# Performance work log

Hardware: AMD Instinct MI355X
Metric: run time of the kernel (lower is better)

The kernel has to match this reference:

```python
import jax, jax.numpy as jnp
import numpy as np

B, Dx, Dz, Dy, H = 4096, 512, 512, 256, 2048
T0, T1 = 0.0, 1.0
N_STEPS = 64


def setup_inputs() -> dict:
    key = jax.random.key(0)
    ks = jax.random.split(key, 9)
    X = jax.random.normal(ks[0], (B, Dx), jnp.float32)
    # P sampled Uniform(0.01, 0.1) as in the torch module
    P = jax.random.uniform(ks[1], (Dz, Dx), jnp.float32, 0.01, 0.1)
    # A scaled so spectral radius ~1 -> exp(A*T) stays bounded over the integration
    A = jax.random.normal(ks[2], (Dz, Dz), jnp.float32) * (Dz ** -0.5)
    W1 = jax.random.normal(ks[3], (H, Dz), jnp.float32) * (Dz ** -0.5)
    b1 = jax.random.normal(ks[4], (H,), jnp.float32) * 0.01
    W2 = jax.random.normal(ks[5], (H, H), jnp.float32) * (H ** -0.5)
    b2 = jax.random.normal(ks[6], (H,), jnp.float32) * 0.01
    W3 = jax.random.normal(ks[7], (Dy, H), jnp.float32) * (H ** -0.5)
    b3 = jax.random.normal(ks[8], (Dy,), jnp.float32) * 0.01
    return dict(X=X, P=P, A=A, W1=W1, b1=b1, W2=W2, b2=b2, W3=W3, b3=b3,
                n_steps=N_STEPS)


def reference(X, P, A, W1, b1, W2, b2, W3, b3, n_steps):
    # Z0 = einsum('ji,bi->bj', P, X)  -> projection into latent ODE state
    z0 = X @ P.T  # [B, Dz]
    dt = jnp.float32((T1 - T0) / n_steps)

    def f(z):  # dz/dt = A z, batched: einsum('ji,bi->bj', A, z)
        return z @ A.T

    def rk4_step(z, _):
        k1 = f(z)
        k2 = f(z + 0.5 * dt * k1)
        k3 = f(z + 0.5 * dt * k2)
        k4 = f(z + dt * k3)
        return z + (dt / 6.0) * (k1 + 2.0 * k2 + 2.0 * k3 + k4), None

    zT, _ = jax.lax.scan(rk4_step, z0, None, length=n_steps)  # [B, Dz]

    # QnnMatrixODE MLP head (n_layers=3): Lin+ReLU, Lin+ReLU, Lin
    h = jax.nn.relu(zT @ W1.T + b1)
    h = jax.nn.relu(h @ W2.T + b2)
    y = h @ W3.T + b3  # [B, Dy]
    return y
```

## Files before the change

### kernel.cpp

```cpp
#include <hip/hip_runtime.h>

#define BDIM 4096
#define DX 512
#define DZ 512
#define DY 256
#define HD 2048
#define LDT 72

typedef __attribute__((ext_vector_type(8))) short bf16x8;
typedef __attribute__((ext_vector_type(4))) float f32x4;

__device__ inline unsigned short f2bf(float f) {
    unsigned u = __float_as_uint(f);
    unsigned r = 0x7FFFu + ((u >> 16) & 1u);
    return (unsigned short)((u + r) >> 16);
}
__device__ inline float bf2f(unsigned short h) {
    return __uint_as_float(((unsigned)h) << 16);
}

#define GLDS16(g, l)                                                            \
    __builtin_amdgcn_global_load_lds((const __attribute__((address_space(1))) void*)(g), \
                                     (__attribute__((address_space(3))) void*)(l), 16, 0, 0)

struct CvtJobs {
    const float* src[5];
    unsigned short* hi[5];
    unsigned short* lo[5];
    int n4[5];
};
__global__ __launch_bounds__(256) void cvt_multi_k(CvtJobs J) {
    const int j = blockIdx.y;
    const int i4 = blockIdx.x * 256 + threadIdx.x;
    if (i4 >= J.n4[j]) return;
    float4 v = ((const float4*)J.src[j])[i4];
    ushort4 h;
    h.x = f2bf(v.x); h.y = f2bf(v.y); h.z = f2bf(v.z); h.w = f2bf(v.w);
    ((ushort4*)J.hi[j])[i4] = h;
    if (J.lo[j]) {
        ushort4 l;
        l.x = f2bf(v.x - bf2f(h.x));
        l.y = f2bf(v.y - bf2f(h.y));
        l.z = f2bf(v.z - bf2f(h.z));
        l.w = f2bf(v.w - bf2f(h.w));
        ((ushort4*)J.lo[j])[i4] = l;
    }
}

__global__ __launch_bounds__(256) void split_t_k(const float* __restrict__ A0,
                                                 unsigned short* __restrict__ H0,
                                                 unsigned short* __restrict__ L0,
                                                 const float* __restrict__ A1,
                                                 unsigned short* __restrict__ H1,
                                                 unsigned short* __restrict__ L1, int D) {
    const float* A = blockIdx.z ? A1 : A0;
    unsigned short* HT = blockIdx.z ? H1 : H0;
    unsigned short* LT = blockIdx.z ? L1 : L0;
    __shared__ float t[32][33];
    const int bx = blockIdx.x * 32, by = blockIdx.y * 32;
    const int x = threadIdx.x, y = threadIdx.y;
#pragma unroll
    for (int dy = 0; dy < 32; dy += 8)
        t[y + dy][x] = A[(size_t)(by + y + dy) * D + bx + x];
    __syncthreads();
#pragma unroll
    for (int dy = 0; dy < 32; dy += 8) {
        float v = t[x][y + dy];
        unsigned short h = f2bf(v);
        size_t o = (size_t)(bx + y + dy) * D + by + x;
        HT[o] = h;
        LT[o] = f2bf(v - bf2f(h));
    }
}

__global__ __launch_bounds__(256) void e0_k(const float* __restrict__ A,
                                            const float* __restrict__ A2,
                                            const float* __restrict__ A3,
                                            float* __restrict__ B0,
                                            float* __restrict__ B1,
                                            float* __restrict__ B2,
                                            unsigned short* __restrict__ B3h,
                                            unsigned short* __restrict__ B3l) {
    const int i4 = blockIdx.x * 256 + threadIdx.x;
    const int base = i4 * 4;
    const int row = base >> 9, col = base & 511;
    const int d = row - col;
    float4 a = ((const float4*)A)[i4];
    float4 a2 = ((const float4*)A2)[i4];
    float4 a3 = ((const float4*)A3)[i4];
    float av[4] = {a.x, a.y, a.z, a.w};
    float a2v[4] = {a2.x, a2.y, a2.z, a2.w};
    float a3v[4] = {a3.x, a3.y, a3.z, a3.w};
    float b0[4], b1[4], b2[4];
    ushort4 h3, l3;
    unsigned short* h3p = &h3.x;
    unsigned short* l3p = &l3.x;
#pragma unroll
    for (int j = 0; j < 4; ++j) {
        const float di = (j == d) ? 1.0f : 0.0f;
        b0[j] = di + av[j] + 0.5f * a2v[j] + 1.6666667e-1f * a3v[j];
        b1[j] = 4.1666668e-2f * di + 8.3333333e-3f * av[j] +
                1.3888889e-3f * a2v[j] + 1.9841270e-4f * a3v[j];
        b2[j] = 2.4801587e-5f * di + 2.7557319e-6f * av[j] +
                2.7557319e-7f * a2v[j] + 2.5052108e-8f * a3v[j];
        float b3 = 2.0876757e-9f * di + 1.6059044e-10f * av[j] +
                   1.1470746e-11f * a2v[j] + 7.6471637e-13f * a3v[j];
        unsigned short hh = f2bf(b3);
        h3p[j] = hh;
        l3p[j] = f2bf(b3 - bf2f(hh));
    }
    ((float4*)B0)[i4] = make_float4(b0[0], b0[1], b0[2], b0[3]);
    ((float4*)B1)[i4] = make_float4(b1[0], b1[1], b1[2], b1[3]);
    ((float4*)B2)[i4] = make_float4(b2[0], b2[1], b2[2], b2[3]);
    ((ushort4*)B3h)[i4] = h3;
    ((ushort4*)B3l)[i4] = l3;
}

struct G64In { const unsigned short *Ahi, *Alo, *Bhi, *Blo; const float* Dadd; };
struct G64Out { float* Cf32; unsigned short *Chi, *Clo, *CThi, *CTlo; };

__device__ __forceinline__ void g64_core(int bx, int by, int M, int N, int K,
                                         G64In in, G64Out o,
                                         unsigned short* Ash, unsigned short* Asl,
                                         unsigned short* Bsh, unsigned short* Bsl) {
    const int tid = threadIdx.x;
    const int lane = tid & 63;
    const int wave = tid >> 6;
    const int wr = wave >> 1, wc = wave & 1;
    const int row0 = by * 64, col0 = bx * 64;
    const int sr = tid >> 2;
    const int sk = (tid & 3) * 16;

    const int niter = K >> 6;
    bf16x8 pa0, pa1, pl0, pl1, pb0, pb1, pq0, pq1;
    {
        const unsigned short* ar = in.Ahi + (size_t)(row0 + sr) * K + sk;
        const unsigned short* al = in.Alo + (size_t)(row0 + sr) * K + sk;
        const unsigned short* br = in.Bhi + (size_t)(col0 + sr) * K + sk;
        const unsigned short* bl = in.Blo + (size_t)(col0 + sr) * K + sk;
        pa0 = *(const bf16x8*)ar; pa1 = *(const bf16x8*)(ar + 8);
        pl0 = *(const bf16x8*)al; pl1 = *(const bf16x8*)(al + 8);
        pb0 = *(const bf16x8*)br; pb1 = *(const bf16x8*)(br + 8);
        pq0 = *(const bf16x8*)bl; pq1 = *(const bf16x8*)(bl + 8);
    }

    f32x4 acc[4] = {};
    const int mb = wr * 32 + (lane & 15);
    const int nb = wc * 32 + (lane & 15);

    for (int it = 0; it < niter; ++it) {
        __syncthreads();
        *(bf16x8*)&Ash[sr * LDT + sk] = pa0; *(bf16x8*)&Ash[sr * LDT + sk + 8] = pa1;
        *(bf16x8*)&Asl[sr * LDT + sk] = pl0; *(bf16x8*)&Asl[sr * LDT + sk + 8] = pl1;
        *(bf16x8*)&Bsh[sr * LDT + sk] = pb0; *(bf16x8*)&Bsh[sr * LDT + sk + 8] = pb1;
        *(bf16x8*)&Bsl[sr * LDT + sk] = pq0; *(bf16x8*)&Bsl[sr * LDT + sk + 8] = pq1;
        __syncthreads();

        {
            const int kn = (it + 1 < niter) ? ((it + 1) << 6) : 0;
            const unsigned short* ar = in.Ahi + (size_t)(row0 + sr) * K + kn + sk;
            const unsigned short* al = in.Alo + (size_t)(row0 + sr) * K + kn + sk;
            const unsigned short* br = in.Bhi + (size_t)(col0 + sr) * K + kn + sk;
            const unsigned short* bl = in.Blo + (size_t)(col0 + sr) * K + kn + sk;
            pa0 = *(const bf16x8*)ar; pa1 = *(const bf16x8*)(ar + 8);
            pl0 = *(const bf16x8*)al; pl1 = *(const bf16x8*)(al + 8);
            pb0 = *(const bf16x8*)br; pb1 = *(const bf16x8*)(br + 8);
            pq0 = *(const bf16x8*)bl; pq1 = *(const bf16x8*)(bl + 8);
        }

#pragma unroll
        for (int kh = 0; kh < 2; ++kh) {
            const int kk = kh * 32 + (lane >> 4) * 8;
            bf16x8 ah[2], alx[2], bh[2], blx[2];
#pragma unroll
            for (int t = 0; t < 2; ++t) {
                ah[t]  = *(const bf16x8*)&Ash[(mb + t * 16) * LDT + kk];
                alx[t] = *(const bf16x8*)&Asl[(mb + t * 16) * LDT + kk];
                bh[t]  = *(const bf16x8*)&Bsh[(nb + t * 16) * LDT + kk];
                blx[t] = *(const bf16x8*)&Bsl[(nb + t * 16) * LDT + kk];
            }
#pragma unroll
            for (int mt = 0; mt < 2; ++mt)
#pragma unroll
                for (int nt = 0; nt < 2; ++nt) {
                    acc[mt * 2 + nt] = __builtin_amdgcn_mfma_f32_16x16x32_bf16(
                        ah[mt], bh[nt], acc[mt * 2 + nt], 0, 0, 0);
                    acc[mt * 2 + nt] = __builtin_amdgcn_mfma_f32_16x16x32_bf16(
                        ah[mt], blx[nt], acc[mt * 2 + nt], 0, 0, 0);
                    acc[mt * 2 + nt] = __builtin_amdgcn_mfma_f32_16x16x32_bf16(
                        alx[mt], bh[nt], acc[mt * 2 + nt], 0, 0, 0);
                }
        }
    }

#pragma unroll
    for (int mt = 0; mt < 2; ++mt) {
        const int grow = row0 + wr * 32 + mt * 16 + (lane >> 4) * 4;
#pragma unroll
        for (int nt = 0; nt < 2; ++nt) {
            const int gcol = col0 + wc * 32 + nt * 16 + (lane & 15);
            f32x4 a = acc[mt * 2 + nt];
            if (in.Dadd) {
#pragma unroll
                for (int i = 0; i < 4; ++i)
                    a[i] += in.Dadd[(size_t)(grow + i) * N + gcol];
            }
            unsigned short h4[4], l4[4];
#pragma unroll
            for (int i = 0; i < 4; ++i) {
                h4[i] = f2bf(a[i]);
                l4[i] = f2bf(a[i] - bf2f(h4[i]));
            }
            if (o.Cf32) {
#pragma unroll
                for (int i = 0; i < 4; ++i) o.Cf32[(size_t)(grow + i) * N + gcol] = a[i];
            }
            if (o.Chi) {
#pragma unroll
                for (int i = 0; i < 4; ++i) o.Chi[(size_t)(grow + i) * N + gcol] = h4[i];
            }
            if (o.Clo) {
#pragma unroll
                for (int i = 0; i < 4; ++i) o.Clo[(size_t)(grow + i) * N + gcol] = l4[i];
            }
            if (o.CThi) {
                ushort4 u = {h4[0], h4[1], h4[2], h4[3]};
                *(ushort4*)&o.CThi[(size_t)gcol * M + grow] = u;
            }
            if (o.CTlo) {
                ushort4 u = {l4[0], l4[1], l4[2], l4[3]};
                *(ushort4*)&o.CTlo[(size_t)gcol * M + grow] = u;
            }
        }
    }
}

__global__ __launch_bounds__(256) void g64_one(G64In in, G64Out o, int M, int N, int K) {
    __shared__ __align__(16) unsigned short Ash[64 * LDT], Asl[64 * LDT];
    __shared__ __align__(16) unsigned short Bsh[64 * LDT], Bsl[64 * LDT];
    g64_core(blockIdx.x, blockIdx.y, M, N, K, in, o, Ash, Asl, Bsh, Bsl);
}

__global__ __launch_bounds__(256) void g64_dual(G64In i0, G64Out o0, G64In i1, G64Out o1,
                                                int M, int N, int K) {
    __shared__ __align__(16) unsigned short Ash[64 * LDT], Asl[64 * LDT];
    __shared__ __align__(16) unsigned short Bsh[64 * LDT], Bsl[64 * LDT];
    g64_core(blockIdx.x, blockIdx.y, M, N, K, blockIdx.z ? i1 : i0, blockIdx.z ? o1 : o0,
             Ash, Asl, Bsh, Bsl);
}

template <int RELU, int BIAS, int OUT_BF16>
__global__ __launch_bounds__(256) void gemm_bf16_v2(int M, int N, int K,
                                                    const unsigned short* __restrict__ A,
                                                    const unsigned short* __restrict__ B,
                                                    void* __restrict__ C,
                                                    const float* __restrict__ bias) {
    __shared__ unsigned short As[64 * 32];
    __shared__ unsigned short Bs[128 * 32];

    const int tid = threadIdx.x;
    const int lane = tid & 63;
    const int wave = tid >> 6;
    const int wr = wave >> 1, wc = wave & 1;
    const int row0 = blockIdx.y * 64;
    const int col0 = blockIdx.x * 128;

    const int srow = lane >> 2;
    const int schunk = (lane & 3) * 8;

    f32x4 acc[2][4] = {};

    for (int k0 = 0; k0 < K; k0 += 32) {
        GLDS16(A + (size_t)(row0 + wave * 16 + srow) * K + k0 + schunk, &As[(wave * 16) * 32]);
        GLDS16(B + (size_t)(col0 + wave * 32 + srow) * K + k0 + schunk, &Bs[(wave * 32) * 32]);
        GLDS16(B + (size_t)(col0 + wave * 32 + 16 + srow) * K + k0 + schunk,
               &Bs[(wave * 32 + 16) * 32]);
        __syncthreads();

        const int kk = (lane >> 4) * 8;
        const int mbase = wr * 32 + (lane & 15);
        const int nbase = wc * 64 + (lane & 15);
        bf16x8 af[2], bf[4];
#pragma unroll
        for (int t = 0; t < 2; ++t) af[t] = *(const bf16x8*)&As[(mbase + t * 16) * 32 + kk];
#pragma unroll
        for (int t = 0; t < 4; ++t) bf[t] = *(const bf16x8*)&Bs[(nbase + t * 16) * 32 + kk];
#pragma unroll
        for (int mt = 0; mt < 2; ++mt)
#pragma unroll
            for (int nt = 0; nt < 4; ++nt)
                acc[mt][nt] = __builtin_amdgcn_mfma_f32_16x16x32_bf16(af[mt], bf[nt],
                                                                      acc[mt][nt], 0, 0, 0);
        __syncthreads();
    }

#pragma unroll
    for (int mt = 0; mt < 2; ++mt) {
        const int grow = row0 + wr * 32 + mt * 16 + (lane >> 4) * 4;
#pragma unroll
        for (int nt = 0; nt < 4; ++nt) {
            const int gcol = col0 + wc * 64 + nt * 16 + (lane & 15);
            const float bv = BIAS ? bias[gcol] : 0.0f;
#pragma unroll
            for (int i = 0; i < 4; ++i) {
                float v = acc[mt][nt][i] + bv;
                if (RELU) v = fmaxf(v, 0.0f);
                const size_t off = (size_t)(grow + i) * N + gcol;
                if (OUT_BF16)
                    ((unsigned short*)C)[off] = f2bf(v);
                else
                    ((float*)C)[off] = v;
            }
        }
    }
}

__global__ __launch_bounds__(256) void gemm64nt_y(int M, int N, int K,
                                                  const unsigned short* __restrict__ A,
                                                  const unsigned short* __restrict__ B,
                                                  float* __restrict__ C,
                                                  const float* __restrict__ bias) {
    __shared__ __align__(16) unsigned short As[64 * LDT];
    __shared__ __align__(16) unsigned short Bs[64 * LDT];
    const int tid = threadIdx.x;
    const int lane = tid & 63;
    const int wave = tid >> 6;
    const int wr = wave >> 1, wc = wave & 1;
    const int row0 = blockIdx.y * 64;
    const int col0 = blockIdx.x * 64;
    const int sr = tid >> 2, sk = (tid & 3) * 16;

    const int niter = K >> 6;
    bf16x8 pa0, pa1, pb0, pb1;
    {
        const unsigned short* ar = A + (size_t)(row0 + sr) * K + sk;
        const unsigned short* br = B + (size_t)(col0 + sr) * K + sk;
        pa0 = *(const bf16x8*)ar; pa1 = *(const bf16x8*)(ar + 8);
        pb0 = *(const bf16x8*)br; pb1 = *(const bf16x8*)(br + 8);
    }

    f32x4 acc[4] = {};
    const int mb = wr * 32 + (lane & 15);
    const int nb = wc * 32 + (lane & 15);

    for (int it = 0; it < niter; ++it) {
        __syncthreads();
        *(bf16x8*)&As[sr * LDT + sk] = pa0; *(bf16x8*)&As[sr * LDT + sk + 8] = pa1;
        *(bf16x8*)&Bs[sr * LDT + sk] = pb0; *(bf16x8*)&Bs[sr * LDT + sk + 8] = pb1;
        __syncthreads();

        {
            const int kn = (it + 1 < niter) ? ((it + 1) << 6) : 0;
            const unsigned short* ar = A + (size_t)(row0 + sr) * K + kn + sk;
            const unsigned short* br = B + (size_t)(col0 + sr) * K + kn + sk;
            pa0 = *(const bf16x8*)ar; pa1 = *(const bf16x8*)(ar + 8);
            pb0 = *(const bf16x8*)br; pb1 = *(const bf16x8*)(br + 8);
        }

#pragma unroll
        for (int kh = 0; kh < 2; ++kh) {
            const int kk = kh * 32 + (lane >> 4) * 8;
            bf16x8 af[2], bf[2];
#pragma unroll
            for (int t = 0; t < 2; ++t) {
                af[t] = *(const bf16x8*)&As[(mb + t * 16) * LDT + kk];
                bf[t] = *(const bf16x8*)&Bs[(nb + t * 16) * LDT + kk];
            }
#pragma unroll
            for (int mt = 0; mt < 2; ++mt)
#pragma unroll
                for (int nt = 0; nt < 2; ++nt)
                    acc[mt * 2 + nt] = __builtin_amdgcn_mfma_f32_16x16x32_bf16(
                        af[mt], bf[nt], acc[mt * 2 + nt], 0, 0, 0);
        }
    }

#pragma unroll
    for (int mt = 0; mt < 2; ++mt) {
        const int grow = row0 + wr * 32 + mt * 16 + (lane >> 4) * 4;
#pragma unroll
        for (int nt = 0; nt < 2; ++nt) {
            const int gcol = col0 + wc * 32 + nt * 16 + (lane & 15);
            const float bv = bias ? bias[gcol] : 0.0f;
#pragma unroll
            for (int i = 0; i < 4; ++i)
                C[(size_t)(grow + i) * N + gcol] = acc[mt * 2 + nt][i] + bv;
        }
    }
}

extern "C" void kernel_launch(void* const* d_in, const int* in_sizes, int n_in,
                              void* d_out, int out_size, void* d_ws, size_t ws_size,
                              hipStream_t stream) {
    const float* X  = (const float*)d_in[0];
    const float* P  = (const float*)d_in[1];
    const float* Am = (const float*)d_in[2];
    const float* W1 = (const float*)d_in[3];
    const float* b1 = (const float*)d_in[4];
    const float* W2 = (const float*)d_in[5];
    const float* b2 = (const float*)d_in[6];
    const float* W3 = (const float*)d_in[7];
    const float* b3 = (const float*)d_in[8];
    float* out = (float*)d_out;

    const size_t S = (size_t)DZ * DZ;

    char* p = (char*)d_ws;
    auto alloc_f = [&](size_t n) { float* r = (float*)p; p += n * 4; return r; };
    auto alloc_h = [&](size_t n) { unsigned short* r = (unsigned short*)p; p += ((n * 2 + 15) & ~15ull); return r; };
    unsigned short* Xb   = alloc_h((size_t)BDIM * DX);
    unsigned short* W2b  = alloc_h((size_t)HD * HD);
    unsigned short* W3b  = alloc_h((size_t)DY * HD);
    unsigned short* W1h  = alloc_h((size_t)HD * DZ);
    unsigned short* W1l  = alloc_h((size_t)HD * DZ);
    unsigned short* Ah   = alloc_h(S);
    unsigned short* Al   = alloc_h(S);
    unsigned short* ATh  = alloc_h(S);
    unsigned short* ATl  = alloc_h(S);
    unsigned short* PTh  = alloc_h(S);
    unsigned short* PTl  = alloc_h(S);
    float* A2f = alloc_f(S);
    float* A3f = alloc_f(S);
    unsigned short* A2h  = alloc_h(S);
    unsigned short* A2l  = alloc_h(S);
    unsigned short* A2Th = alloc_h(S);
    unsigned short* A2Tl = alloc_h(S);
    unsigned short* A4Th = alloc_h(S);
    unsigned short* A4Tl = alloc_h(S);
    float* B0f = alloc_f(S);
    float* B1f = alloc_f(S);
    float* B2f = alloc_f(S);
    unsigned short* B3h  = alloc_h(S);
    unsigned short* B3l  = alloc_h(S);
    unsigned short* H1h  = alloc_h(S);
    unsigned short* H1l  = alloc_h(S);
    unsigned short* H2h  = alloc_h(S);
    unsigned short* H2l  = alloc_h(S);
    unsigned short* H3h  = alloc_h(S);
    unsigned short* H3l  = alloc_h(S);
    unsigned short* RTh  = alloc_h(S);
    unsigned short* RTl  = alloc_h(S);
    unsigned short* C1b  = alloc_h((size_t)HD * DZ);
    unsigned short* h1b  = alloc_h((size_t)BDIM * HD);
    unsigned short* h2b  = alloc_h((size_t)BDIM * HD);

    CvtJobs J;
    J.src[0] = X;  J.hi[0] = Xb;  J.lo[0] = nullptr; J.n4[0] = BDIM * DX / 4;
    J.src[1] = W2; J.hi[1] = W2b; J.lo[1] = nullptr; J.n4[1] = HD * HD / 4;
    J.src[2] = W3; J.hi[2] = W3b; J.lo[2] = nullptr; J.n4[2] = DY * HD / 4;
    J.src[3] = W1; J.hi[3] = W1h; J.lo[3] = W1l;     J.n4[3] = HD * DZ / 4;
    J.src[4] = Am; J.hi[4] = Ah;  J.lo[4] = Al;      J.n4[4] = (int)(S / 4);
    cvt_multi_k<<<dim3(HD * HD / 4 / 256, 5), 256, 0, stream>>>(J);

    split_t_k<<<dim3(DZ / 32, DZ / 32, 2), dim3(32, 8), 0, stream>>>(
        Am, ATh, ATl, P, PTh, PTl, DZ);

    dim3 g8(DZ / 64, DZ / 64);

    {
        G64In i{Ah, Al, ATh, ATl, nullptr};
        G64Out o{A2f, A2h, A2l, A2Th, A2Tl};
        g64_one<<<g8, 256, 0, stream>>>(i, o, DZ, DZ, DZ);
    }
    {
        G64In i0{A2h, A2l, ATh, ATl, nullptr};
        G64Out o0{A3f, nullptr, nullptr, nullptr, nullptr};
        G64In i1{A2h, A2l, A2Th, A2Tl, nullptr};
        G64Out o1{nullptr, nullptr, nullptr, A4Th, A4Tl};
        g64_dual<<<dim3(DZ / 64, DZ / 64, 2), 256, 0, stream>>>(i0, o0, i1, o1, DZ, DZ, DZ);
    }
    e0_k<<<dim3((int)(S / 4 / 256)), 256, 0, stream>>>(Am, A2f, A3f, B0f, B1f, B2f, B3h, B3l);

    {
        G64In i{B3h, B3l, A4Th, A4Tl, B2f};
        G64Out o{nullptr, H1h, H1l, nullptr, nullptr};
        g64_one<<<g8, 256, 0, stream>>>(i, o, DZ, DZ, DZ);
    }
    {
        G64In i{H1h, H1l, A4Th, A4Tl, B1f};
        G64Out o{nullptr, H2h, H2l, nullptr, nullptr};
        g64_one<<<g8, 256, 0, stream>>>(i, o, DZ, DZ, DZ);
    }
    {
        G64In i{H2h, H2l, A4Th, A4Tl, B0f};
        G64Out o{nullptr, H3h, H3l, nullptr, nullptr};
        g64_one<<<g8, 256, 0, stream>>>(i, o, DZ, DZ, DZ);
    }
    {
        G64In i{H3h, H3l, PTh, PTl, nullptr};
        G64Out o{nullptr, nullptr, nullptr, RTh, RTl};
        g64_one<<<g8, 256, 0, stream>>>(i, o, DZ, DZ, DZ);
    }
    {
        G64In i{W1h, W1l, RTh, RTl, nullptr};
        G64Out o{nullptr, C1b, nullptr, nullptr, nullptr};
        g64_one<<<dim3(DZ / 64, HD / 64), 256, 0, stream>>>(i, o, HD, DZ, DZ);
    }

    gemm_bf16_v2<1, 1, 1><<<dim3(HD / 128, BDIM / 64), 256, 0, stream>>>(
        BDIM, HD, DX, Xb, C1b, h1b, b1);
    gemm_bf16_v2<1, 1, 1><<<dim3(HD / 128, BDIM / 64), 256, 0, stream>>>(
        BDIM, HD, HD, h1b, W2b, h2b, b2);
    gemm64nt_y<<<dim3(DY / 64, BDIM / 64), 256, 0, stream>>>(
        BDIM, DY, HD, h2b, W3b, out, b3);
}
```

Measured before the change: 267.3 us.

## Fuse prep kernels and e0 epilogue, project X through P up front

The transpose-split of A moves into the conversion kernel as an extra job. The elementwise e0 polynomial-coefficient kernel becomes a templated epilogue of the A^3 GEMM, so A2/A3 are no longer stored in fp32. The separate H3·P^T GEMM is removed: X is first projected with a bf16 GEMM against P, and the propagator is applied to that projection instead. This cuts kernel launches and intermediate traffic, but computes X·P^T and stores its result in single bf16 (P has no lo part), which lowers precision.

After: 268.3 us. About the same (+0.4%).

```diff
diff --git a/kernel.cpp b/kernel.cpp
--- a/kernel.cpp
+++ b/kernel.cpp
@@ -23,104 +23,64 @@
     __builtin_amdgcn_global_load_lds((const __attribute__((address_space(1))) void*)(g), \
                                      (__attribute__((address_space(3))) void*)(l), 16, 0, 0)
 
-struct CvtJobs {
-    const float* src[5];
-    unsigned short* hi[5];
-    unsigned short* lo[5];
-    int n4[5];
+struct PrepJobs {
+    const float* src[7];
+    unsigned short* hi[7];
+    unsigned short* lo[7];
+    int n4[7];
 };
-__global__ __launch_bounds__(256) void cvt_multi_k(CvtJobs J) {
+__global__ __launch_bounds__(256) void prep_k(PrepJobs J) {
     const int j = blockIdx.y;
-    const int i4 = blockIdx.x * 256 + threadIdx.x;
-    if (i4 >= J.n4[j]) return;
-    float4 v = ((const float4*)J.src[j])[i4];
-    ushort4 h;
-    h.x = f2bf(v.x); h.y = f2bf(v.y); h.z = f2bf(v.z); h.w = f2bf(v.w);
-    ((ushort4*)J.hi[j])[i4] = h;
-    if (J.lo[j]) {
-        ushort4 l;
-        l.x = f2bf(v.x - bf2f(h.x));
-        l.y = f2bf(v.y - bf2f(h.y));
-        l.z = f2bf(v.z - bf2f(h.z));
-        l.w = f2bf(v.w - bf2f(h.w));
-        ((ushort4*)J.lo[j])[i4] = l;
-    }
-}
-
-__global__ __launch_bounds__(256) void split_t_k(const float* __restrict__ A0,
-                                                 unsigned short* __restrict__ H0,
-                                                 unsigned short* __restrict__ L0,
-                                                 const float* __restrict__ A1,
-                                                 unsigned short* __restrict__ H1,
-                                                 unsigned short* __restrict__ L1, int D) {
-    const float* A = blockIdx.z ? A1 : A0;
-    unsigned short* HT = blockIdx.z ? H1 : H0;
-    unsigned short* LT = blockIdx.z ? L1 : L0;
-    __shared__ float t[32][33];
-    const int bx = blockIdx.x * 32, by = blockIdx.y * 32;
-    const int x = threadIdx.x, y = threadIdx.y;
-#pragma unroll
-    for (int dy = 0; dy < 32; dy += 8)
-        t[y + dy][x] = A[(size_t)(by + y + dy) * D + bx + x];
-    __syncthreads();
-#pragma unroll
-    for (int dy = 0; dy < 32; dy += 8) {
-        float v = t[x][y + dy];
-        unsigned short h = f2bf(v);
-        size_t o = (size_t)(bx + y + dy) * D + by + x;
-        HT[o] = h;
-        LT[o] = f2bf(v - bf2f(h));
-    }
-}
-
-__global__ __launch_bounds__(256) void e0_k(const float* __restrict__ A,
-                                            const float* __restrict__ A2,
-                                            const float* __restrict__ A3,
-                                            float* __restrict__ B0,
-                                            float* __restrict__ B1,
-                                            float* __restrict__ B2,
-                                            unsigned short* __restrict__ B3h,
-                                            unsigned short* __restrict__ B3l) {
-    const int i4 = blockIdx.x * 256 + threadIdx.x;
-    const int base = i4 * 4;
-    const int row = base >> 9, col = base & 511;
-    const int d = row - col;
-    float4 a = ((const float4*)A)[i4];
-    float4 a2 = ((const float4*)A2)[i4];
-    float4 a3 = ((const float4*)A3)[i4];
-    float av[4] = {a.x, a.y, a.z, a.w};
-    float a2v[4] = {a2.x, a2.y, a2.z, a2.w};
-    float a3v[4] = {a3.x, a3.y, a3.z, a3.w};
-    float b0[4], b1[4], b2[4];
-    ushort4 h3, l3;
-    unsigned short* h3p = &h3.x;
-    unsigned short* l3p = &l3.x;
-#pragma unroll
-    for (int j = 0; j < 4; ++j) {
-        const float di = (j == d) ? 1.0f : 0.0f;
-        b0[j] = di + av[j] + 0.5f * a2v[j] + 1.6666667e-1f * a3v[j];
-        b1[j] = 4.1666668e-2f * di + 8.3333333e-3f * av[j] +
-                1.3888889e-3f * a2v[j] + 1.9841270e-4f * a3v[j];
-        b2[j] = 2.4801587e-5f * di + 2.7557319e-6f * av[j] +
-                2.7557319e-7f * a2v[j] + 2.5052108e-8f * a3v[j];
-        float b3 = 2.0876757e-9f * di + 1.6059044e-10f * av[j] +
-                   1.1470746e-11f * a2v[j] + 7.6471637e-13f * a3v[j];
-        unsigned short hh = f2bf(b3);
-        h3p[j] = hh;
-        l3p[j] = f2bf(b3 - bf2f(hh));
-    }
-    ((float4*)B0)[i4] = make_float4(b0[0], b0[1], b0[2], b0[3]);
-    ((float4*)B1)[i4] = make_float4(b1[0], b1[1], b1[2], b1[3]);
-    ((float4*)B2)[i4] = make_float4(b2[0], b2[1], b2[2], b2[3]);
-    ((ushort4*)B3h)[i4] = h3;
-    ((ushort4*)B3l)[i4] = l3;
+    if (j < 6) {
+        const int i4 = blockIdx.x * 256 + threadIdx.x;
+        if (i4 >= J.n4[j]) return;
+        float4 v = ((const float4*)J.src[j])[i4];
+        ushort4 h;
+        h.x = f2bf(v.x); h.y = f2bf(v.y); h.z = f2bf(v.z); h.w = f2bf(v.w);
+        ((ushort4*)J.hi[j])[i4] = h;
+        if (J.lo[j]) {
+            ushort4 l;
+            l.x = f2bf(v.x - bf2f(h.x));
+            l.y = f2bf(v.y - bf2f(h.y));
+            l.z = f2bf(v.z - bf2f(h.z));
+            l.w = f2bf(v.w - bf2f(h.w));
+            ((ushort4*)J.lo[j])[i4] = l;
+        }
+    } else {
+        if (blockIdx.x >= 256) return;
+        __shared__ float t[32][33];
+        const float* A = J.src[6];
+        unsigned short* HT = J.hi[6];
+        unsigned short* LT = J.lo[6];
+        const int bx = (blockIdx.x & 15) * 32, by = (blockIdx.x >> 4) * 32;
+        const int x = threadIdx.x & 31, y = threadIdx.x >> 5;
+#pragma unroll
+        for (int dy = 0; dy < 32; dy += 8)
+            t[y + dy][x] = A[(size_t)(by + y + dy) * DZ + bx + x];
+        __syncthreads();
+#pragma unroll
+        for (int dy = 0; dy < 32; dy += 8) {
+            float v = t[x][y + dy];
+            unsigned short h = f2bf(v);
+            size_t o = (size_t)(bx + y + dy) * DZ + by + x;
+            HT[o] = h;
+            LT[o] = f2bf(v - bf2f(h));
+        }
+    }
 }
 
 struct G64In { const unsigned short *Ahi, *Alo, *Bhi, *Blo; const float* Dadd; };
 struct G64Out { float* Cf32; unsigned short *Chi, *Clo, *CThi, *CTlo; };
-
+struct E0Out {
+    const float* Af32;
+    const unsigned short *A2h, *A2l;
+    float *B0, *B1, *B2;
+    unsigned short *B3h, *B3l;
+};
+
+template <int EPI>
 __device__ __forceinline__ void g64_core(int bx, int by, int M, int N, int K,
-                                         G64In in, G64Out o,
+                                         G64In in, G64Out o, E0Out e,
                                          unsigned short* Ash, unsigned short* Asl,
                                          unsigned short* Bsh, unsigned short* Bsl) {
     const int tid = threadIdx.x;
@@ -200,36 +160,57 @@
         for (int nt = 0; nt < 2; ++nt) {
             const int gcol = col0 + wc * 32 + nt * 16 + (lane & 15);
             f32x4 a = acc[mt * 2 + nt];
-            if (in.Dadd) {
-#pragma unroll
-                for (int i = 0; i < 4; ++i)
-                    a[i] += in.Dadd[(size_t)(grow + i) * N + gcol];
-            }
-            unsigned short h4[4], l4[4];
-#pragma unroll
-            for (int i = 0; i < 4; ++i) {
-                h4[i] = f2bf(a[i]);
-                l4[i] = f2bf(a[i] - bf2f(h4[i]));
-            }
-            if (o.Cf32) {
-#pragma unroll
-                for (int i = 0; i < 4; ++i) o.Cf32[(size_t)(grow + i) * N + gcol] = a[i];
-            }
-            if (o.Chi) {
-#pragma unroll
-                for (int i = 0; i < 4; ++i) o.Chi[(size_t)(grow + i) * N + gcol] = h4[i];
-            }
-            if (o.Clo) {
-#pragma unroll
-                for (int i = 0; i < 4; ++i) o.Clo[(size_t)(grow + i) * N + gcol] = l4[i];
-            }
-            if (o.CThi) {
-                ushort4 u = {h4[0], h4[1], h4[2], h4[3]};
-                *(ushort4*)&o.CThi[(size_t)gcol * M + grow] = u;
-            }
-            if (o.CTlo) {
-                ushort4 u = {l4[0], l4[1], l4[2], l4[3]};
-                *(ushort4*)&o.CTlo[(size_t)gcol * M + grow] = u;
+            if (EPI == 1) {
+#pragma unroll
+                for (int i = 0; i < 4; ++i) {
+                    const size_t idx = (size_t)(grow + i) * N + gcol;
+                    const float di = (grow + i == gcol) ? 1.0f : 0.0f;
+                    const float av = e.Af32[idx];
+                    const float a2v = bf2f(e.A2h[idx]) + bf2f(e.A2l[idx]);
+                    const float a3v = a[i];
+                    e.B0[idx] = di + av + 0.5f * a2v + 1.6666667e-1f * a3v;
+                    e.B1[idx] = 4.1666668e-2f * di + 8.3333333e-3f * av +
+                                1.3888889e-3f * a2v + 1.9841270e-4f * a3v;
+                    e.B2[idx] = 2.4801587e-5f * di + 2.7557319e-6f * av +
+                                2.7557319e-7f * a2v + 2.5052108e-8f * a3v;
+                    float b3 = 2.0876757e-9f * di + 1.6059044e-10f * av +
+                               1.1470746e-11f * a2v + 7.6471637e-13f * a3v;
+                    unsigned short hh = f2bf(b3);
+                    e.B3h[idx] = hh;
+                    e.B3l[idx] = f2bf(b3 - bf2f(hh));
+                }
+            } else {
+                if (in.Dadd) {
+#pragma unroll
+                    for (int i = 0; i < 4; ++i)
+                        a[i] += in.Dadd[(size_t)(grow + i) * N + gcol];
+                }
+                unsigned short h4[4], l4[4];
+#pragma unroll
+                for (int i = 0; i < 4; ++i) {
+                    h4[i] = f2bf(a[i]);
+                    l4[i] = f2bf(a[i] - bf2f(h4[i]));
+                }
+                if (o.Cf32) {
+#pragma unroll
+                    for (int i = 0; i < 4; ++i) o.Cf32[(size_t)(grow + i) * N + gcol] = a[i];
+                }
+                if (o.Chi) {
+#pragma unroll
+                    for (int i = 0; i < 4; ++i) o.Chi[(size_t)(grow + i) * N + gcol] = h4[i];
+                }
+                if (o.Clo) {
+#pragma unroll
+                    for (int i = 0; i < 4; ++i) o.Clo[(size_t)(grow + i) * N + gcol] = l4[i];
+                }
+                if (o.CThi) {
+                    ushort4 u = {h4[0], h4[1], h4[2], h4[3]};
+                    *(ushort4*)&o.CThi[(size_t)gcol * M + grow] = u;
+                }
+                if (o.CTlo) {
+                    ushort4 u = {l4[0], l4[1], l4[2], l4[3]};
+                    *(ushort4*)&o.CTlo[(size_t)gcol * M + grow] = u;
+                }
             }
         }
     }
@@ -238,15 +219,21 @@
 __global__ __launch_bounds__(256) void g64_one(G64In in, G64Out o, int M, int N, int K) {
     __shared__ __align__(16) unsigned short Ash[64 * LDT], Asl[64 * LDT];
     __shared__ __align__(16) unsigned short Bsh[64 * LDT], Bsl[64 * LDT];
-    g64_core(blockIdx.x, blockIdx.y, M, N, K, in, o, Ash, Asl, Bsh, Bsl);
-}
-
-__global__ __launch_bounds__(256) void g64_dual(G64In i0, G64Out o0, G64In i1, G64Out o1,
-                                                int M, int N, int K) {
+    E0Out e = {};
+    g64_core<0>(blockIdx.x, blockIdx.y, M, N, K, in, o, e, Ash, Asl, Bsh, Bsl);
+}
+
+__global__ __launch_bounds__(256) void g64_dual_e0(G64In i0, E0Out e0o,
+                                                   G64In i1, G64Out o1) {
     __shared__ __align__(16) unsigned short Ash[64 * LDT], Asl[64 * LDT];
     __shared__ __align__(16) unsigned short Bsh[64 * LDT], Bsl[64 * LDT];
-    g64_core(blockIdx.x, blockIdx.y, M, N, K, blockIdx.z ? i1 : i0, blockIdx.z ? o1 : o0,
-             Ash, Asl, Bsh, Bsl);
+    if (blockIdx.z == 0) {
+        G64Out on = {};
+        g64_core<1>(blockIdx.x, blockIdx.y, DZ, DZ, DZ, i0, on, e0o, Ash, Asl, Bsh, Bsl);
+    } else {
+        E0Out en = {};
+        g64_core<0>(blockIdx.x, blockIdx.y, DZ, DZ, DZ, i1, o1, en, Ash, Asl, Bsh, Bsl);
+    }
 }
 
 template <int RELU, int BIAS, int OUT_BF16>
@@ -413,14 +400,11 @@
     unsigned short* W3b  = alloc_h((size_t)DY * HD);
     unsigned short* W1h  = alloc_h((size_t)HD * DZ);
     unsigned short* W1l  = alloc_h((size_t)HD * DZ);
+    unsigned short* Pb   = alloc_h(S);
     unsigned short* Ah   = alloc_h(S);
     unsigned short* Al   = alloc_h(S);
     unsigned short* ATh  = alloc_h(S);
     unsigned short* ATl  = alloc_h(S);
-    unsigned short* PTh  = alloc_h(S);
-    unsigned short* PTl  = alloc_h(S);
-    float* A2f = alloc_f(S);
-    float* A3f = alloc_f(S);
     unsigned short* A2h  = alloc_h(S);
     unsigned short* A2l  = alloc_h(S);
     unsigned short* A2Th = alloc_h(S);
@@ -436,41 +420,40 @@
     unsigned short* H1l  = alloc_h(S);
     unsigned short* H2h  = alloc_h(S);
     unsigned short* H2l  = alloc_h(S);
-    unsigned short* H3h  = alloc_h(S);
-    unsigned short* H3l  = alloc_h(S);
-    unsigned short* RTh  = alloc_h(S);
-    unsigned short* RTl  = alloc_h(S);
+    unsigned short* H3Th = alloc_h(S);
+    unsigned short* H3Tl = alloc_h(S);
     unsigned short* C1b  = alloc_h((size_t)HD * DZ);
+    unsigned short* XPb  = alloc_h((size_t)BDIM * DZ);
     unsigned short* h1b  = alloc_h((size_t)BDIM * HD);
     unsigned short* h2b  = alloc_h((size_t)BDIM * HD);
 
-    CvtJobs J;
+    PrepJobs J;
     J.src[0] = X;  J.hi[0] = Xb;  J.lo[0] = nullptr; J.n4[0] = BDIM * DX / 4;
     J.src[1] = W2; J.hi[1] = W2b; J.lo[1] = nullptr; J.n4[1] = HD * HD / 4;
     J.src[2] = W3; J.hi[2] = W3b; J.lo[2] = nullptr; J.n4[2] = DY * HD / 4;
     J.src[3] = W1; J.hi[3] = W1h; J.lo[3] = W1l;     J.n4[3] = HD * DZ / 4;
     J.src[4] = Am; J.hi[4] = Ah;  J.lo[4] = Al;      J.n4[4] = (int)(S / 4);
-    cvt_multi_k<<<dim3(HD * HD / 4 / 256, 5), 256, 0, stream>>>(J);
-
-    split_t_k<<<dim3(DZ / 32, DZ / 32, 2), dim3(32, 8), 0, stream>>>(
-        Am, ATh, ATl, P, PTh, PTl, DZ);
+    J.src[5] = P;  J.hi[5] = Pb;  J.lo[5] = nullptr; J.n4[5] = (int)(S / 4);
+    J.src[6] = Am; J.hi[6] = ATh; J.lo[6] = ATl;     J.n4[6] = 256;
+    prep_k<<<dim3(HD * HD / 4 / 256, 7), 256, 0, stream>>>(J);
+
+    gemm_bf16_v2<0, 0, 1><<<dim3(DZ / 128, BDIM / 64), 256, 0, stream>>>(
+        BDIM, DZ, DX, Xb, Pb, XPb, nullptr);
 
     dim3 g8(DZ / 64, DZ / 64);
 
     {
         G64In i{Ah, Al, ATh, ATl, nullptr};
-        G64Out o{A2f, A2h, A2l, A2Th, A2Tl};
+        G64Out o{nullptr, A2h, A2l, A2Th, A2Tl};
         g64_one<<<g8, 256, 0, stream>>>(i, o, DZ, DZ, DZ);
     }
     {
         G64In i0{A2h, A2l, ATh, ATl, nullptr};
-        G64Out o0{A3f, nullptr, nullptr, nullptr, nullptr};
+        E0Out e0o{Am, A2h, A2l, B0f, B1f, B2f, B3h, B3l};
         G64In i1{A2h, A2l, A2Th, A2Tl, nullptr};
         G64Out o1{nullptr, nullptr, nullptr, A4Th, A4Tl};
-        g64_dual<<<dim3(DZ / 64, DZ / 64, 2), 256, 0, stream>>>(i0, o0, i1, o1, DZ, DZ, DZ);
-    }
-    e0_k<<<dim3((int)(S / 4 / 256)), 256, 0, stream>>>(Am, A2f, A3f, B0f, B1f, B2f, B3h, B3l);
-
+        g64_dual_e0<<<dim3(DZ / 64, DZ / 64, 2), 256, 0, stream>>>(i0, e0o, i1, o1);
+    }
     {
         G64In i{B3h, B3l, A4Th, A4Tl, B2f};
         G64Out o{nullptr, H1h, H1l, nullptr, nullptr};
@@ -483,22 +466,17 @@
     }
     {
         G64In i{H2h, H2l, A4Th, A4Tl, B0f};
-        G64Out o{nullptr, H3h, H3l, nullptr, nullptr};
+        G64Out o{nullptr, nullptr, nullptr, H3Th, H3Tl};
         g64_one<<<g8, 256, 0, stream>>>(i, o, DZ, DZ, DZ);
     }
     {
-        G64In i{H3h, H3l, PTh, PTl, nullptr};
-        G64Out o{nullptr, nullptr, nullptr, RTh, RTl};
-        g64_one<<<g8, 256, 0, stream>>>(i, o, DZ, DZ, DZ);
-    }
-    {
-        G64In i{W1h, W1l, RTh, RTl, nullptr};
+        G64In i{W1h, W1l, H3Th, H3Tl, nullptr};
         G64Out o{nullptr, C1b, nullptr, nullptr, nullptr};
         g64_one<<<dim3(DZ / 64, HD / 64), 256, 0, stream>>>(i, o, HD, DZ, DZ);
     }
 
     gemm_bf16_v2<1, 1, 1><<<dim3(HD / 128, BDIM / 64), 256, 0, stream>>>(
-        BDIM, HD, DX, Xb, C1b, h1b, b1);
+        BDIM, HD, DZ, XPb, C1b, h1b, b1);
     gemm_bf16_v2<1, 1, 1><<<dim3(HD / 128, BDIM / 64), 256, 0, stream>>>(
         BDIM, HD, HD, h1b, W2b, h2b, b2);
     gemm64nt_y<<<dim3(DY / 64, BDIM / 64), 256, 0, stream>>>(
```
